# Optimization experiments

Hardware: AMD Instinct MI355X
Metric: run time of the kernel (lower is better)

## Reference

```python
import jax, jax.numpy as jnp
import numpy as np

B, S, IN_DIM, OUT_DIM = 4, 4096, 512, 64


def setup_inputs() -> dict:
    key = jax.random.key(0)
    ks = jax.random.split(key, 8)
    scale = 1.0 / np.sqrt(IN_DIM)
    return {
        "input_embedding": jax.random.normal(ks[0], (B, S, IN_DIM), dtype=jnp.float32),
        "mask": jax.random.randint(ks[1], (S, S), 0, 2, dtype=jnp.int32),
        "Wq": jax.random.uniform(ks[2], (IN_DIM, OUT_DIM), jnp.float32, -scale, scale),
        "bq": jax.random.uniform(ks[3], (OUT_DIM,), jnp.float32, -scale, scale),
        "Wk": jax.random.uniform(ks[4], (IN_DIM, OUT_DIM), jnp.float32, -scale, scale),
        "bk": jax.random.uniform(ks[5], (OUT_DIM,), jnp.float32, -scale, scale),
        "Wv": jax.random.uniform(ks[6], (IN_DIM, OUT_DIM), jnp.float32, -scale, scale),
        "bv": jax.random.uniform(ks[7], (OUT_DIM,), jnp.float32, -scale, scale),
    }


def reference(input_embedding, mask, Wq, bq, Wk, bk, Wv, bv):
    # q,k,v: [B,S,D]
    q = jnp.einsum("bsi,id->bsd", input_embedding, Wq) + bq
    k = jnp.einsum("bsi,id->bsd", input_embedding, Wk) + bk
    v = jnp.einsum("bsi,id->bsd", input_embedding, Wv) + bv
    d_k = q.shape[-1]
    # scores: [B,S,S]
    scores = jnp.einsum("bqd,bkd->bqk", q, k) / jnp.sqrt(jnp.float32(d_k))
    # NOTE: original uses masked_fill(mask==0, 1e-6) on the SCORES (not -inf)
    scores = jnp.where(mask == 0, jnp.float32(1e-6), scores)
    probs = jax.nn.softmax(scores, axis=-1)
    return jnp.einsum("bqk,bkd->bqd", probs, v)
```

## Files before the change

### kernel.cpp

```cpp
#include <hip/hip_runtime.h>

#define BATCH 4
#define SEQ 4096
#define IND 512
#define DH 64
#define NSPLIT 8

typedef __attribute__((ext_vector_type(8))) _Float16 f16x8;
typedef __attribute__((ext_vector_type(4))) _Float16 f16x4;
typedef __attribute__((ext_vector_type(4))) float f32x4;
typedef unsigned long long u64;
typedef unsigned int u32;

#define MFMA16(a, b, c) __builtin_amdgcn_mfma_f32_16x16x32_f16(a, b, c, 0, 0, 0)
#define GLL16(g, l)                                                                  \
    __builtin_amdgcn_global_load_lds(                                                \
        (const __attribute__((address_space(1))) void*)(g),                          \
        (__attribute__((address_space(3))) void*)(l), 16, 0, 0)

__global__ __launch_bounds__(256) void mask_row_kernel(const int* __restrict__ mask,
                                                       u64* __restrict__ bits3) {
    const int w = threadIdx.x >> 6, lane = threadIdx.x & 63;
    const int q = blockIdx.x * 4 + w;
    const int* mp = mask + (size_t)q * SEQ + lane;
    int v[64];
#pragma unroll
    for (int kw = 0; kw < 64; ++kw) v[kw] = mp[kw * 64];
#pragma unroll
    for (int kw = 0; kw < 64; ++kw) {
        u64 b = __ballot(v[kw] != 0);
        if (lane == 0) bits3[((size_t)kw << 12) + q] = b;
    }
}

__global__ __launch_bounds__(256) void wprep_kernel(
    const float* __restrict__ Wq, const float* __restrict__ bq,
    const float* __restrict__ Wk, const float* __restrict__ bk,
    const float* __restrict__ Wv, const float* __restrict__ bv,
    _Float16* __restrict__ Wt, float* __restrict__ bcat) {
    __shared__ float tile[64][65];
    const int bid = blockIdx.x, tid = threadIdx.x;
    const int mat = bid >> 3, k0 = (bid & 7) * 64;
    const float QS = 0.125f * 1.44269504088896f;
    const float* W = (mat == 0) ? Wq : ((mat == 1) ? Wk : Wv);
    const float scale = (mat == 0) ? QS : 1.0f;
    if (bid == 0 && tid < 192) {
        int m2 = tid >> 6, n = tid & 63;
        const float* bb = (m2 == 0) ? bq : ((m2 == 1) ? bk : bv);
        bcat[tid] = bb[n] * ((m2 == 0) ? QS : 1.0f);
    }
    const int n = tid & 63, r0 = tid >> 6;
#pragma unroll
    for (int i = 0; i < 16; ++i) {
        int r = r0 * 16 + i;
        tile[r][n] = W[(size_t)(k0 + r) * 64 + n];
    }
    __syncthreads();
    const int k = tid & 63, n0 = tid >> 6;
#pragma unroll
    for (int i = 0; i < 16; ++i) {
        int nn = n0 * 16 + i;
        Wt[(size_t)(mat * 64 + nn) * IND + k0 + k] = (_Float16)(tile[k][nn] * scale);
    }
}

__global__ __launch_bounds__(192) void qkv_kernel(const float* __restrict__ X,
    const _Float16* __restrict__ Wt, const float* __restrict__ bcat,
    _Float16* __restrict__ Qh, _Float16* __restrict__ Kh, _Float16* __restrict__ Vt) {
    __shared__ __align__(16) _Float16 xs[32 * 520];
    const int tid = threadIdx.x;
    const int w = tid >> 6, lane = tid & 63, l15 = lane & 15, g = lane >> 4;
    const int m0 = blockIdx.x * 32;

    const float4* src = (const float4*)(X + (size_t)m0 * IND);
#pragma unroll
    for (int u = 0; u < 22; ++u) {
        int idx = u * 192 + tid;
        if (idx < 4096) {
            float4 x = src[idx];
            int row = idx >> 7, c4 = idx & 127;
            f16x4 h;
            h[0] = (_Float16)x.x; h[1] = (_Float16)x.y;
            h[2] = (_Float16)x.z; h[3] = (_Float16)x.w;
            *(f16x4*)&xs[row * 520 + c4 * 4] = h;
        }
    }
    __syncthreads();

    f32x4 acc0[4], acc1[4];
#pragma unroll
    for (int nt = 0; nt < 4; ++nt) {
        acc0[nt] = (f32x4){0.f, 0.f, 0.f, 0.f};
        acc1[nt] = (f32x4){0.f, 0.f, 0.f, 0.f};
    }

    const _Float16* Wm = Wt + (size_t)(w * 64 + l15) * IND + g * 8;
#pragma unroll
    for (int kc = 0; kc < 16; ++kc) {
        f16x8 a0 = *(const f16x8*)&xs[l15 * 520 + kc * 32 + g * 8];
        f16x8 a1 = *(const f16x8*)&xs[(16 + l15) * 520 + kc * 32 + g * 8];
#pragma unroll
        for (int nt = 0; nt < 4; ++nt) {
            f16x8 wf = *(const f16x8*)(Wm + kc * 32 + (size_t)nt * 16 * IND);
            acc0[nt] = MFMA16(a0, wf, acc0[nt]);
            acc1[nt] = MFMA16(a1, wf, acc1[nt]);
        }
    }

    const int b = m0 >> 12;
    const int sbase = m0 & (SEQ - 1);
#pragma unroll
    for (int nt = 0; nt < 4; ++nt) {
        float bias = bcat[w * 64 + nt * 16 + l15];
        int ncol = nt * 16 + l15;
        if (w == 0) {
#pragma unroll
            for (int r = 0; r < 4; ++r) {
                Qh[(size_t)(m0 + g * 4 + r) * DH + ncol] = (_Float16)(acc0[nt][r] + bias);
                Qh[(size_t)(m0 + 16 + g * 4 + r) * DH + ncol] = (_Float16)(acc1[nt][r] + bias);
            }
        } else if (w == 1) {
#pragma unroll
            for (int r = 0; r < 4; ++r) {
                Kh[(size_t)(m0 + g * 4 + r) * DH + ncol] = (_Float16)(acc0[nt][r] + bias);
                Kh[(size_t)(m0 + 16 + g * 4 + r) * DH + ncol] = (_Float16)(acc1[nt][r] + bias);
            }
        } else {
            f16x4 v0, v1;
#pragma unroll
            for (int r = 0; r < 4; ++r) {
                v0[r] = (_Float16)(acc0[nt][r] + bias);
                v1[r] = (_Float16)(acc1[nt][r] + bias);
            }
            _Float16* vb = Vt + ((size_t)b * DH + ncol) * SEQ + sbase + 8 * g;
            *(f16x4*)(vb) = v0;
            *(f16x4*)(vb + 4) = v1;
        }
    }
}

__global__ __launch_bounds__(256, 2) void flash_kernel(
    const _Float16* __restrict__ Qh, const _Float16* __restrict__ Kh,
    const _Float16* __restrict__ Vt, const u64* __restrict__ bits3,
    float* __restrict__ accP, float* __restrict__ lP) {
    constexpr int KPWT = SEQ / NSPLIT;
    constexpr int NT = KPWT / 64;
    __shared__ __align__(16) _Float16 ks[2][64 * 64];
    __shared__ __align__(16) _Float16 vs[2][64 * 64];

    const int tid = threadIdx.x;
    const int w = tid >> 6, lane = tid & 63, l15 = lane & 15, g = lane >> 4;
    const int bid = blockIdx.x;
    const int xcd = bid & 7, i = bid >> 3;
    const int b = xcd >> 1;
    const int split = (xcd & 1) * 4 + (i & 3);
    const int qblk = i >> 2;
    const int q0 = qblk * 256 + w * 64;
    const int k0base = split * KPWT;

    const _Float16* Qb = Qh + (size_t)b * SEQ * DH;
    const _Float16* Kb = Kh + (size_t)b * SEQ * DH;
    const _Float16* Vb = Vt + (size_t)b * DH * SEQ;
    const u64* bitsQ = bits3 + q0;

    const int tau = w * 1024 + lane * 16;
    const size_t vg0 = (size_t)(tau >> 7) * (SEQ * 2) + (tau & 127);
    _Float16* kl0 = &ks[0][w * 512];
    _Float16* kl1 = &ks[1][w * 512];
    _Float16* vl0 = &vs[0][w * 512];
    _Float16* vl1 = &vs[1][w * 512];

    f16x8 Qa[4][2];
#pragma unroll
    for (int mi = 0; mi < 4; ++mi)
#pragma unroll
        for (int kc = 0; kc < 2; ++kc)
            Qa[mi][kc] = *(const f16x8*)(Qb + (size_t)(q0 + mi * 16 + l15) * DH + kc * 32 + g * 8);

    f32x4 O[4][4];
    float lsum[4];
#pragma unroll
    for (int mi = 0; mi < 4; ++mi)
#pragma unroll
        for (int nd = 0; nd < 4; ++nd) O[mi][nd] = (f32x4){0.f, 0.f, 0.f, 0.f};
#pragma unroll
    for (int j = 0; j < 4; ++j) lsum[j] = 0.f;

    {
        const char* kg = (const char*)Kb + (size_t)k0base * 128 + tau;
        const char* vg = (const char*)Vb + vg0 + (size_t)k0base * 2;
        GLL16(kg, kl0);
        GLL16(kg + 4096, kl0 + 2048);
        GLL16(vg, vl0);
        GLL16(vg + (size_t)32 * SEQ * 2, vl0 + 2048);
    }
    __syncthreads();

#pragma unroll 2
    for (int t = 0; t < NT; ++t) {
        const int cur = t & 1;
        const int k0 = k0base + t * 64;
        const int kw = k0 >> 6;
        if (t + 1 < NT) {
            const char* kg = (const char*)Kb + (size_t)(k0 + 64) * 128 + tau;
            const char* vg = (const char*)Vb + vg0 + (size_t)(k0 + 64) * 2;
            _Float16* kl = cur ? kl0 : kl1;
            _Float16* vl = cur ? vl0 : vl1;
            GLL16(kg, kl);
            GLL16(kg + 4096, kl + 2048);
            GLL16(vg, vl);
            GLL16(vg + (size_t)32 * SEQ * 2, vl + 2048);
        }

        f16x8 Kf[4][2], Vf[4][2];
#pragma unroll
        for (int kk = 0; kk < 4; ++kk)
#pragma unroll
            for (int kc = 0; kc < 2; ++kc)
                Kf[kk][kc] = *(const f16x8*)&ks[cur][(kk * 16 + l15) * 64 + kc * 32 + g * 8];
#pragma unroll
        for (int nd = 0; nd < 4; ++nd)
#pragma unroll
            for (int h = 0; h < 2; ++h)
                Vf[nd][h] = *(const f16x8*)&vs[cur][(nd * 16 + l15) * 64 + h * 32 + g * 8];

#pragma unroll
        for (int mi = 0; mi < 4; ++mi) {
            u64 bw = bitsQ[((size_t)kw << 12) + mi * 16 + l15];
            f32x4 c0 = {0.f, 0.f, 0.f, 0.f}, c1 = {0.f, 0.f, 0.f, 0.f};
            f32x4 c2 = {0.f, 0.f, 0.f, 0.f}, c3 = {0.f, 0.f, 0.f, 0.f};
            c0 = MFMA16(Kf[0][0], Qa[mi][0], c0);
            c0 = MFMA16(Kf[0][1], Qa[mi][1], c0);
            c1 = MFMA16(Kf[1][0], Qa[mi][0], c1);
            c1 = MFMA16(Kf[1][1], Qa[mi][1], c1);
            c2 = MFMA16(Kf[2][0], Qa[mi][0], c2);
            c2 = MFMA16(Kf[2][1], Qa[mi][1], c2);
            c3 = MFMA16(Kf[3][0], Qa[mi][0], c3);
            c3 = MFMA16(Kf[3][1], Qa[mi][1], c3);
            u32 ms0 = (u32)(bw >> (4 * g));
            u32 ms1 = (u32)(bw >> (16 + 4 * g));
            u32 ms2 = (u32)(bw >> (32 + 4 * g));
            u32 ms3 = (u32)(bw >> (48 + 4 * g));
            f16x8 Pa0, Pa1;
            float ls = 0.f;
#pragma unroll
            for (int r = 0; r < 4; ++r) {
                float s0 = ((ms0 >> r) & 1u) ? c0[r] : 0.0f;
                float s1 = ((ms1 >> r) & 1u) ? c1[r] : 0.0f;
                float s2 = ((ms2 >> r) & 1u) ? c2[r] : 0.0f;
                float s3 = ((ms3 >> r) & 1u) ? c3[r] : 0.0f;
                float p0 = __builtin_amdgcn_exp2f(s0);
                float p1 = __builtin_amdgcn_exp2f(s1);
                float p2 = __builtin_amdgcn_exp2f(s2);
                float p3 = __builtin_amdgcn_exp2f(s3);
                ls += (p0 + p1) + (p2 + p3);
                Pa0[r] = (_Float16)p0;
                Pa0[r + 4] = (_Float16)p1;
                Pa1[r] = (_Float16)p2;
                Pa1[r + 4] = (_Float16)p3;
            }
            lsum[mi] += ls;
#pragma unroll
            for (int nd = 0; nd < 4; ++nd) {
                O[mi][nd] = MFMA16(Pa0, Vf[nd][0], O[mi][nd]);
                O[mi][nd] = MFMA16(Pa1, Vf[nd][1], O[mi][nd]);
            }
        }
        __syncthreads();
    }

#pragma unroll
    for (int j = 0; j < 4; ++j) {
        float v = lsum[j];
        v += __shfl_xor(v, 16);
        v += __shfl_xor(v, 32);
        lsum[j] = v;
    }
    float* accB = accP + ((size_t)split * BATCH + b) * SEQ * DH;
    float* lB = lP + ((size_t)split * BATCH + b) * SEQ;
    if (lane < 16) {
#pragma unroll
        for (int mi = 0; mi < 4; ++mi)
            lB[q0 + mi * 16 + l15] = lsum[mi];
    }
#pragma unroll
    for (int mi = 0; mi < 4; ++mi)
#pragma unroll
        for (int nd = 0; nd < 4; ++nd)
#pragma unroll
            for (int r = 0; r < 4; ++r)
                accB[(size_t)(q0 + mi * 16 + 4 * g + r) * DH + nd * 16 + l15] = O[mi][nd][r];
}

__global__ __launch_bounds__(256) void reduce_kernel(const float* __restrict__ accP,
                                                     const float* __restrict__ lP,
                                                     float* __restrict__ out) {
    int idx = blockIdx.x * 256 + threadIdx.x;
    int bq = idx >> 6, d = idx & 63;
    float a = 0.f, l = 0.f;
#pragma unroll
    for (int s = 0; s < NSPLIT; ++s) {
        a += accP[((size_t)s * BATCH * SEQ + bq) * DH + d];
        l += lP[(size_t)s * BATCH * SEQ + bq];
    }
    out[idx] = a / l;
}

extern "C" void kernel_launch(void* const* d_in, const int* in_sizes, int n_in,
                              void* d_out, int out_size, void* d_ws, size_t ws_size,
                              hipStream_t stream) {
    const float* X = (const float*)d_in[0];
    const int* mask = (const int*)d_in[1];
    const float* Wq = (const float*)d_in[2];
    const float* bq = (const float*)d_in[3];
    const float* Wk = (const float*)d_in[4];
    const float* bk = (const float*)d_in[5];
    const float* Wv = (const float*)d_in[6];
    const float* bv = (const float*)d_in[7];
    float* out = (float*)d_out;

    char* ws = (char*)d_ws;
    _Float16* Qh = (_Float16*)ws;
    _Float16* Kh = (_Float16*)(ws + (2u << 20));
    _Float16* Vt = (_Float16*)(ws + (4u << 20));
    u64* bits3 = (u64*)(ws + (6u << 20));
    float* accP = (float*)(ws + (8u << 20));
    float* lP = (float*)(ws + (40u << 20));
    _Float16* Wt = (_Float16*)(ws + (41u << 20));
    float* bcat = (float*)(ws + (41u << 20) + (256u << 10));

    mask_row_kernel<<<dim3(1024), dim3(256), 0, stream>>>(mask, bits3);
    wprep_kernel<<<dim3(24), dim3(256), 0, stream>>>(Wq, bq, Wk, bk, Wv, bv, Wt, bcat);
    qkv_kernel<<<dim3(512), dim3(192), 0, stream>>>(X, Wt, bcat, Qh, Kh, Vt);
    flash_kernel<<<dim3(512), dim3(256), 0, stream>>>(Qh, Kh, Vt, bits3, accP, lP);
    reduce_kernel<<<dim3(BATCH * SEQ * DH / 256), dim3(256), 0, stream>>>(accP, lP, out);
}
```

Before: 81.19 us.

## Double key splits, store fp16 partials, merge mask and weight prep kernels

Raises the key-dimension split from 8 to 16, doubling the flash grid to 1024 blocks, and raises the launch bound to 4 blocks per CU so more waves are resident. Partial accumulators are written as fp16 instead of fp32, halving partial-result traffic, and the reduce kernel reads two elements per thread. The mask bit-packing and weight preparation kernels are merged into one launch. The cost is extra partial traffic and reduce work from more splits, possible register pressure from the higher occupancy bound, and some precision loss in fp16 partial sums.

```diff
diff --git a/kernel.cpp b/kernel.cpp
--- a/kernel.cpp
+++ b/kernel.cpp
@@ -4,10 +4,11 @@
 #define SEQ 4096
 #define IND 512
 #define DH 64
-#define NSPLIT 8
+#define NSPLIT 16
 
 typedef __attribute__((ext_vector_type(8))) _Float16 f16x8;
 typedef __attribute__((ext_vector_type(4))) _Float16 f16x4;
+typedef __attribute__((ext_vector_type(2))) _Float16 f16x2;
 typedef __attribute__((ext_vector_type(4))) float f32x4;
 typedef unsigned long long u64;
 typedef unsigned int u32;
@@ -18,28 +19,29 @@
         (const __attribute__((address_space(1))) void*)(g),                          \
         (__attribute__((address_space(3))) void*)(l), 16, 0, 0)
 
-__global__ __launch_bounds__(256) void mask_row_kernel(const int* __restrict__ mask,
-                                                       u64* __restrict__ bits3) {
-    const int w = threadIdx.x >> 6, lane = threadIdx.x & 63;
-    const int q = blockIdx.x * 4 + w;
-    const int* mp = mask + (size_t)q * SEQ + lane;
-    int v[64];
-#pragma unroll
-    for (int kw = 0; kw < 64; ++kw) v[kw] = mp[kw * 64];
-#pragma unroll
-    for (int kw = 0; kw < 64; ++kw) {
-        u64 b = __ballot(v[kw] != 0);
-        if (lane == 0) bits3[((size_t)kw << 12) + q] = b;
-    }
-}
-
-__global__ __launch_bounds__(256) void wprep_kernel(
+__global__ __launch_bounds__(256) void mask_wprep_kernel(const int* __restrict__ mask,
+    u64* __restrict__ bits3,
     const float* __restrict__ Wq, const float* __restrict__ bq,
     const float* __restrict__ Wk, const float* __restrict__ bk,
     const float* __restrict__ Wv, const float* __restrict__ bv,
     _Float16* __restrict__ Wt, float* __restrict__ bcat) {
     __shared__ float tile[64][65];
-    const int bid = blockIdx.x, tid = threadIdx.x;
+    const int tid = threadIdx.x;
+    if (blockIdx.x < 1024) {
+        const int w = tid >> 6, lane = tid & 63;
+        const int q = blockIdx.x * 4 + w;
+        const int* mp = mask + (size_t)q * SEQ + lane;
+        int v[64];
+#pragma unroll
+        for (int kw = 0; kw < 64; ++kw) v[kw] = mp[kw * 64];
+#pragma unroll
+        for (int kw = 0; kw < 64; ++kw) {
+            u64 b = __ballot(v[kw] != 0);
+            if (lane == 0) bits3[((size_t)kw << 12) + q] = b;
+        }
+        return;
+    }
+    const int bid = blockIdx.x - 1024;
     const int mat = bid >> 3, k0 = (bid & 7) * 64;
     const float QS = 0.125f * 1.44269504088896f;
     const float* W = (mat == 0) ? Wq : ((mat == 1) ? Wk : Wv);
@@ -139,10 +141,10 @@
     }
 }
 
-__global__ __launch_bounds__(256, 2) void flash_kernel(
+__global__ __launch_bounds__(256, 4) void flash_kernel(
     const _Float16* __restrict__ Qh, const _Float16* __restrict__ Kh,
     const _Float16* __restrict__ Vt, const u64* __restrict__ bits3,
-    float* __restrict__ accP, float* __restrict__ lP) {
+    _Float16* __restrict__ accP, float* __restrict__ lP) {
     constexpr int KPWT = SEQ / NSPLIT;
     constexpr int NT = KPWT / 64;
     __shared__ __align__(16) _Float16 ks[2][64 * 64];
@@ -153,8 +155,8 @@
     const int bid = blockIdx.x;
     const int xcd = bid & 7, i = bid >> 3;
     const int b = xcd >> 1;
-    const int split = (xcd & 1) * 4 + (i & 3);
-    const int qblk = i >> 2;
+    const int split = (xcd & 1) * 8 + (i & 7);
+    const int qblk = i >> 3;
     const int q0 = qblk * 256 + w * 64;
     const int k0base = split * KPWT;
 
@@ -276,7 +278,7 @@
         v += __shfl_xor(v, 32);
         lsum[j] = v;
     }
-    float* accB = accP + ((size_t)split * BATCH + b) * SEQ * DH;
+    _Float16* accB = accP + ((size_t)split * BATCH + b) * SEQ * DH;
     float* lB = lP + ((size_t)split * BATCH + b) * SEQ;
     if (lane < 16) {
 #pragma unroll
@@ -289,21 +291,26 @@
         for (int nd = 0; nd < 4; ++nd)
 #pragma unroll
             for (int r = 0; r < 4; ++r)
-                accB[(size_t)(q0 + mi * 16 + 4 * g + r) * DH + nd * 16 + l15] = O[mi][nd][r];
-}
-
-__global__ __launch_bounds__(256) void reduce_kernel(const float* __restrict__ accP,
+                accB[(size_t)(q0 + mi * 16 + 4 * g + r) * DH + nd * 16 + l15] =
+                    (_Float16)O[mi][nd][r];
+}
+
+__global__ __launch_bounds__(256) void reduce_kernel(const _Float16* __restrict__ accP,
                                                      const float* __restrict__ lP,
                                                      float* __restrict__ out) {
     int idx = blockIdx.x * 256 + threadIdx.x;
-    int bq = idx >> 6, d = idx & 63;
-    float a = 0.f, l = 0.f;
+    int bq = idx >> 5, d2 = idx & 31;
+    float a0 = 0.f, a1 = 0.f, l = 0.f;
 #pragma unroll
     for (int s = 0; s < NSPLIT; ++s) {
-        a += accP[((size_t)s * BATCH * SEQ + bq) * DH + d];
+        f16x2 v = *(const f16x2*)&accP[((size_t)s * BATCH * SEQ + bq) * DH + d2 * 2];
+        a0 += (float)v[0];
+        a1 += (float)v[1];
         l += lP[(size_t)s * BATCH * SEQ + bq];
     }
-    out[idx] = a / l;
+    float inv = 1.0f / l;
+    float2 o = make_float2(a0 * inv, a1 * inv);
+    *(float2*)&out[(size_t)idx * 2] = o;
 }
 
 extern "C" void kernel_launch(void* const* d_in, const int* in_sizes, int n_in,
@@ -324,14 +331,14 @@
     _Float16* Kh = (_Float16*)(ws + (2u << 20));
     _Float16* Vt = (_Float16*)(ws + (4u << 20));
     u64* bits3 = (u64*)(ws + (6u << 20));
-    float* accP = (float*)(ws + (8u << 20));
+    _Float16* accP = (_Float16*)(ws + (8u << 20));
     float* lP = (float*)(ws + (40u << 20));
     _Float16* Wt = (_Float16*)(ws + (41u << 20));
     float* bcat = (float*)(ws + (41u << 20) + (256u << 10));
 
-    mask_row_kernel<<<dim3(1024), dim3(256), 0, stream>>>(mask, bits3);
-    wprep_kernel<<<dim3(24), dim3(256), 0, stream>>>(Wq, bq, Wk, bk, Wv, bv, Wt, bcat);
+    mask_wprep_kernel<<<dim3(1048), dim3(256), 0, stream>>>(mask, bits3, Wq, bq, Wk, bk,
+                                                            Wv, bv, Wt, bcat);
     qkv_kernel<<<dim3(512), dim3(192), 0, stream>>>(X, Wt, bcat, Qh, Kh, Vt);
-    flash_kernel<<<dim3(512), dim3(256), 0, stream>>>(Qh, Kh, Vt, bits3, accP, lP);
-    reduce_kernel<<<dim3(BATCH * SEQ * DH / 256), dim3(256), 0, stream>>>(accP, lP, out);
-}
+    flash_kernel<<<dim3(1024), dim3(256), 0, stream>>>(Qh, Kh, Vt, bits3, accP, lP);
+    reduce_kernel<<<dim3(BATCH * SEQ * DH / 512), dim3(256), 0, stream>>>(accP, lP, out);
+}
```

New measurement: 264.0 us. +225.1%, slower.
